# Kernel tuning notes

Measured on AMD Instinct MI355X. Metric: run time of the kernel, lower is better.

## Reference

```python
import jax, jax.numpy as jnp
import numpy as np

B, T, V, H = 32, 2048, 64, 256
HD = H // 2  # per-direction hidden (bidirectional GRU)


def setup_inputs() -> dict:
    key = jax.random.key(0)
    ks = jax.random.split(key, 8)
    s = 0.1
    return {
        "tokens": jax.random.randint(ks[0], (B, T), 0, V, dtype=jnp.int32),
        "lengths": jax.random.randint(ks[1], (B,), 1, T + 1, dtype=jnp.int32),
        "emb": jax.random.normal(ks[2], (V, H), jnp.float32) * s,
        "Wih_f": jax.random.normal(ks[3], (3 * HD, H), jnp.float32) * s,
        "Whh_f": jax.random.normal(ks[4], (3 * HD, HD), jnp.float32) * s,
        "bih_f": jnp.zeros((3 * HD,), jnp.float32),
        "bhh_f": jnp.zeros((3 * HD,), jnp.float32),
        "Wih_b": jax.random.normal(ks[5], (3 * HD, H), jnp.float32) * s,
        "Whh_b": jax.random.normal(ks[6], (3 * HD, HD), jnp.float32) * s,
        "bih_b": jnp.zeros((3 * HD,), jnp.float32),
        "bhh_b": jnp.zeros((3 * HD,), jnp.float32),
    }


def _gru_dir(x, mask, Wih, Whh, bih, bhh):
    # x: [B,T,H] inputs, mask: [B,T] valid positions; torch GRU cell math.
    b, t, _ = x.shape
    hd = Whh.shape[1]
    h0 = jnp.zeros((b, hd), x.dtype)

    def step(h, inp):
        x_t, m_t = inp  # [B,H], [B,1]
        gi = x_t @ Wih.T + bih
        gh = h @ Whh.T + bhh
        gi_r, gi_z, gi_n = jnp.split(gi, 3, axis=-1)
        gh_r, gh_z, gh_n = jnp.split(gh, 3, axis=-1)
        r = jax.nn.sigmoid(gi_r + gh_r)
        z = jax.nn.sigmoid(gi_z + gh_z)
        n = jnp.tanh(gi_n + r * gh_n)
        h_new = (1 - z) * n + z * h
        h = jnp.where(m_t, h_new, h)  # freeze state past sequence end
        return h, h

    _, outs = jax.lax.scan(step, h0, (x.transpose(1, 0, 2), mask.T[:, :, None]))
    return outs.transpose(1, 0, 2)  # [B,T,HD]


def reference(tokens, lengths, emb, Wih_f, Whh_f, bih_f, bhh_f, Wih_b, Whh_b, bih_b, bhh_b):
    lengths = jnp.maximum(lengths, 1)
    x = emb[tokens]  # [B,T,H] embedding lookup
    t_idx = jnp.arange(tokens.shape[1])
    mask = t_idx[None, :] < lengths[:, None]  # [B,T]
    # forward direction
    out_f = _gru_dir(x, mask, Wih_f, Whh_f, bih_f, bhh_f)
    # backward direction: reverse each sequence within its valid region
    ridx = jnp.clip(lengths[:, None] - 1 - t_idx[None, :], 0)  # [B,T]
    x_rev = jnp.take_along_axis(x, ridx[:, :, None], axis=1)
    out_b_rev = _gru_dir(x_rev, mask, Wih_b, Whh_b, bih_b, bhh_b)
    out_b = jnp.take_along_axis(out_b_rev, ridx[:, :, None], axis=1)
    out = jnp.concatenate([out_f, out_b], axis=-1)  # [B,T,H] (torch concat order: fwd, bwd)
    # mean pool over valid timesteps (matches .mean(0) per variable-length sequence)
    denom = lengths[:, None].astype(out.dtype)
    pooled = (out * mask[:, :, None]).sum(axis=1) / denom  # [B,H]
    return pooled
```

## Files before the change

### kernel.cpp

```cpp
#include <hip/hip_runtime.h>

#define BB 32
#define TT 2048
#define VV 64
#define HH 256
#define HD 128
#define G3 384

typedef _Float16 h2 __attribute__((ext_vector_type(2)));
typedef _Float16 h8 __attribute__((ext_vector_type(8)));

__device__ __forceinline__ float fsigmoid(float x) {
  return __builtin_amdgcn_rcpf(1.0f + __expf(-x));
}
__device__ __forceinline__ float ftanh(float x) {
  float ax = fabsf(x);
  float t = __expf(-2.0f * ax);
  float r = 1.0f - 2.0f * t * __builtin_amdgcn_rcpf(1.0f + t);
  return copysignf(r, x);
}

__device__ __forceinline__ float quad_reduce_add(float v) {
  int x = __builtin_amdgcn_mov_dpp(__float_as_int(v), 0xB1, 0xF, 0xF, true);
  v += __int_as_float(x);
  x = __builtin_amdgcn_mov_dpp(__float_as_int(v), 0x4E, 0xF, 0xF, true);
  v += __int_as_float(x);
  return v;
}

template <int D>
__device__ __forceinline__ h2 getpair(h8 v) {
  return __builtin_shufflevector(v, v, 2 * D, 2 * D + 1);
}

__global__ __launch_bounds__(G3, 1)
void gi_table_kernel(const float* __restrict__ emb,
                     const float* __restrict__ Wih_f, const float* __restrict__ bih_f,
                     const float* __restrict__ Wih_b, const float* __restrict__ bih_b,
                     float* __restrict__ gi_ws) {
  const int gid = blockIdx.x;
  const int dir = gid >> 6;
  const int v   = gid & 63;
  const int j   = threadIdx.x;
  const float* Wih = dir ? Wih_b : Wih_f;
  const float* bih = dir ? bih_b : bih_f;
  const float4* er = reinterpret_cast<const float4*>(emb + v * HH);
  const float4* wr = reinterpret_cast<const float4*>(Wih + j * HH);
  float acc = bih[j];
  #pragma unroll 8
  for (int k = 0; k < HH / 4; ++k) {
    float4 e = er[k];
    float4 w = wr[k];
    acc = fmaf(e.x, w.x, acc);
    acc = fmaf(e.y, w.y, acc);
    acc = fmaf(e.z, w.z, acc);
    acc = fmaf(e.w, w.w, acc);
  }
  gi_ws[dir * (VV * G3) + v * G3 + j] = acc;
}

__global__ __launch_bounds__(512, 2)
void gru_kernel(const int* __restrict__ tokens, const int* __restrict__ lengths,
                const float* __restrict__ Whh_f, const float* __restrict__ bhh_f,
                const float* __restrict__ Whh_b, const float* __restrict__ bhh_b,
                const float* __restrict__ gi_ws, float* __restrict__ out) {
  __shared__ float giL[VV * G3];
  __shared__ int   tokL[TT];
  __shared__ __align__(16) _Float16 hbufh[2][HD];

  const int bid  = blockIdx.x;
  const int b    = bid & 31;
  const int dir  = bid >> 5;
  const int tid  = threadIdx.x;
  const int wave = tid >> 6;
  const int lane = tid & 63;
  const int quad = lane >> 2;
  const int p    = lane & 3;
  const int i    = wave * 16 + quad;

  int len = lengths[b];
  if (len < 1) len = 1;

  const float* gi_src = gi_ws + dir * (VV * G3);
  for (int idx = tid; idx < VV * G3; idx += 512) giL[idx] = gi_src[idx];
  const int* tb = tokens + b * TT;
  for (int s = tid; s < len; s += 512) tokL[s] = tb[dir ? (len - 1 - s) : s];
  if (tid < HD) hbufh[0][tid] = (_Float16)0.0f;

  const float* Whh = dir ? Whh_b : Whh_f;
  const float* bhh = dir ? bhh_b : bhh_f;
  h8 w8[3][4];
  #pragma unroll
  for (int g = 0; g < 3; ++g) {
    const float* wr = Whh + (g * HD + i) * HD + p * 32;
    #pragma unroll
    for (int c = 0; c < 4; ++c) {
      const int kb = ((c + p) & 3) * 8;
      h8 w;
      #pragma unroll
      for (int d = 0; d < 8; ++d) w[d] = (_Float16)wr[kb + d];
      w8[g][c] = w;
    }
  }
  const float bhr = bhh[i], bhz = bhh[HD + i], bhn = bhh[2 * HD + i];

  __syncthreads();

  float h = 0.0f, hsum = 0.0f;

  int tok = tokL[0];
  float gir = giL[tok * G3 + i];
  float giz = giL[tok * G3 + HD + i];
  float gin = giL[tok * G3 + 2 * HD + i];

#define DOT8(acc, wv, hv)                                            \
  acc = __builtin_amdgcn_fdot2(getpair<0>(wv), getpair<0>(hv), acc, false); \
  acc = __builtin_amdgcn_fdot2(getpair<1>(wv), getpair<1>(hv), acc, false); \
  acc = __builtin_amdgcn_fdot2(getpair<2>(wv), getpair<2>(hv), acc, false); \
  acc = __builtin_amdgcn_fdot2(getpair<3>(wv), getpair<3>(hv), acc, false)

  #pragma unroll 2
  for (int s = 0; s < len; ++s) {
    const int cur = s & 1;
    const h8* hb8 = reinterpret_cast<const h8*>(&hbufh[cur][0]);

    float accr = bhr, accz = bhz, accn = bhn;
    #pragma unroll
    for (int c = 0; c < 4; ++c) {
      const h8 hv = hb8[p * 4 + ((c + p) & 3)];
      DOT8(accr, w8[0][c], hv);
      DOT8(accz, w8[1][c], hv);
      DOT8(accn, w8[2][c], hv);
    }

    const int sn = (s + 1 < len) ? (s + 1) : 0;
    const int ntok = tokL[sn];
    const float ngir = giL[ntok * G3 + i];
    const float ngiz = giL[ntok * G3 + HD + i];
    const float ngin = giL[ntok * G3 + 2 * HD + i];

    accr = quad_reduce_add(accr);
    accz = quad_reduce_add(accz);
    accn = quad_reduce_add(accn);

    const float r = fsigmoid(gir + accr);
    const float z = fsigmoid(giz + accz);
    const float n = ftanh(gin + r * accn);
    h = (1.0f - z) * n + z * h;
    hsum += h;
    if (p == 0) hbufh[cur ^ 1][i] = (_Float16)h;
    __syncthreads();

    gir = ngir; giz = ngiz; gin = ngin;
  }
#undef DOT8

  if (p == 0) out[b * HH + dir * HD + i] = hsum / (float)len;
}

extern "C" void kernel_launch(void* const* d_in, const int* in_sizes, int n_in,
                              void* d_out, int out_size, void* d_ws, size_t ws_size,
                              hipStream_t stream) {
  const int*   tokens  = (const int*)d_in[0];
  const int*   lengths = (const int*)d_in[1];
  const float* emb     = (const float*)d_in[2];
  const float* Wih_f   = (const float*)d_in[3];
  const float* Whh_f   = (const float*)d_in[4];
  const float* bih_f   = (const float*)d_in[5];
  const float* bhh_f   = (const float*)d_in[6];
  const float* Wih_b   = (const float*)d_in[7];
  const float* Whh_b   = (const float*)d_in[8];
  const float* bih_b   = (const float*)d_in[9];
  const float* bhh_b   = (const float*)d_in[10];
  float* out   = (float*)d_out;
  float* gi_ws = (float*)d_ws;

  gi_table_kernel<<<2 * VV, G3, 0, stream>>>(emb, Wih_f, bih_f, Wih_b, bih_b, gi_ws);
  gru_kernel<<<2 * BB, 512, 0, stream>>>(tokens, lengths, Whh_f, bhh_f, Whh_b, bhh_b,
                                         gi_ws, out);
}
```

Measured before the change: 949.7 us.

## Halve GRU block to 256 threads, two hidden units per quad, prescaled exp2 activations

Each lane quad now computes two hidden units, so the recurrent block shrinks from 512 to 256 threads (4 waves), which makes the per-step barrier cheaper and doubles register-held weights per lane. Input-gate tables, recurrent weights and biases are prescaled by -log2(e) or 2·log2(e), so sigmoid and tanh become raw exp2 plus rcp without extra multiplies. The next-token gate prefetch is pipelined one step further ahead. The cost is twice the dot-product work per lane on the serial critical path and higher register pressure.

```diff
diff --git a/kernel.cpp b/kernel.cpp
--- a/kernel.cpp
+++ b/kernel.cpp
@@ -10,15 +10,8 @@
 typedef _Float16 h2 __attribute__((ext_vector_type(2)));
 typedef _Float16 h8 __attribute__((ext_vector_type(8)));
 
-__device__ __forceinline__ float fsigmoid(float x) {
-  return __builtin_amdgcn_rcpf(1.0f + __expf(-x));
-}
-__device__ __forceinline__ float ftanh(float x) {
-  float ax = fabsf(x);
-  float t = __expf(-2.0f * ax);
-  float r = 1.0f - 2.0f * t * __builtin_amdgcn_rcpf(1.0f + t);
-  return copysignf(r, x);
-}
+#define SRZ (-1.4426950408889634f)
+#define SN  (2.8853900817779268f)
 
 __device__ __forceinline__ float quad_reduce_add(float v) {
   int x = __builtin_amdgcn_mov_dpp(__float_as_int(v), 0xB1, 0xF, 0xF, true);
@@ -56,10 +49,11 @@
     acc = fmaf(e.z, w.z, acc);
     acc = fmaf(e.w, w.w, acc);
   }
-  gi_ws[dir * (VV * G3) + v * G3 + j] = acc;
-}
-
-__global__ __launch_bounds__(512, 2)
+  const float sc = (j < 2 * HD) ? SRZ : SN;
+  gi_ws[dir * (VV * G3) + v * G3 + j] = acc * sc;
+}
+
+__global__ __launch_bounds__(256, 1)
 void gru_kernel(const int* __restrict__ tokens, const int* __restrict__ lengths,
                 const float* __restrict__ Whh_f, const float* __restrict__ bhh_f,
                 const float* __restrict__ Whh_b, const float* __restrict__ bhh_b,
@@ -76,44 +70,53 @@
   const int lane = tid & 63;
   const int quad = lane >> 2;
   const int p    = lane & 3;
-  const int i    = wave * 16 + quad;
+  const int q    = wave * 16 + quad;
+  const int i0   = 2 * q;
 
   int len = lengths[b];
   if (len < 1) len = 1;
 
   const float* gi_src = gi_ws + dir * (VV * G3);
-  for (int idx = tid; idx < VV * G3; idx += 512) giL[idx] = gi_src[idx];
+  for (int idx = tid; idx < VV * G3; idx += 256) giL[idx] = gi_src[idx];
   const int* tb = tokens + b * TT;
-  for (int s = tid; s < len; s += 512) tokL[s] = tb[dir ? (len - 1 - s) : s];
+  for (int s = tid; s < len; s += 256) tokL[s] = tb[dir ? (len - 1 - s) : s];
   if (tid < HD) hbufh[0][tid] = (_Float16)0.0f;
 
   const float* Whh = dir ? Whh_b : Whh_f;
   const float* bhh = dir ? bhh_b : bhh_f;
-  h8 w8[3][4];
+  h8 w8[3][2][4];
   #pragma unroll
   for (int g = 0; g < 3; ++g) {
-    const float* wr = Whh + (g * HD + i) * HD + p * 32;
+    const float sc = (g < 2) ? SRZ : SN;
     #pragma unroll
-    for (int c = 0; c < 4; ++c) {
-      const int kb = ((c + p) & 3) * 8;
-      h8 w;
+    for (int o = 0; o < 2; ++o) {
+      const float* wr = Whh + (g * HD + i0 + o) * HD + p * 32;
       #pragma unroll
-      for (int d = 0; d < 8; ++d) w[d] = (_Float16)wr[kb + d];
-      w8[g][c] = w;
+      for (int c = 0; c < 4; ++c) {
+        const int kb = ((c + p) & 3) * 8;
+        h8 w;
+        #pragma unroll
+        for (int d = 0; d < 8; ++d) w[d] = (_Float16)(wr[kb + d] * sc);
+        w8[g][o][c] = w;
+      }
     }
   }
-  const float bhr = bhh[i], bhz = bhh[HD + i], bhn = bhh[2 * HD + i];
+  const float bhr0 = bhh[i0] * SRZ,          bhr1 = bhh[i0 + 1] * SRZ;
+  const float bhz0 = bhh[HD + i0] * SRZ,     bhz1 = bhh[HD + i0 + 1] * SRZ;
+  const float bhn0 = bhh[2 * HD + i0] * SN,  bhn1 = bhh[2 * HD + i0 + 1] * SN;
 
   __syncthreads();
 
-  float h = 0.0f, hsum = 0.0f;
-
-  int tok = tokL[0];
-  float gir = giL[tok * G3 + i];
-  float giz = giL[tok * G3 + HD + i];
-  float gin = giL[tok * G3 + 2 * HD + i];
-
-#define DOT8(acc, wv, hv)                                            \
+  float h0 = 0.0f, h1 = 0.0f, hsum0 = 0.0f, hsum1 = 0.0f;
+
+  const float2* giL2 = reinterpret_cast<const float2*>(giL);
+  int tok0 = tokL[0];
+  float2 gr = giL2[(tok0 * G3) / 2 + q];
+  float2 gz = giL2[(tok0 * G3 + HD) / 2 + q];
+  float2 gn = giL2[(tok0 * G3 + 2 * HD) / 2 + q];
+  int ntok = tokL[(1 < len) ? 1 : 0];
+
+#define DOT8(acc, wv, hv)                                                   \
   acc = __builtin_amdgcn_fdot2(getpair<0>(wv), getpair<0>(hv), acc, false); \
   acc = __builtin_amdgcn_fdot2(getpair<1>(wv), getpair<1>(hv), acc, false); \
   acc = __builtin_amdgcn_fdot2(getpair<2>(wv), getpair<2>(hv), acc, false); \
@@ -124,38 +127,64 @@
     const int cur = s & 1;
     const h8* hb8 = reinterpret_cast<const h8*>(&hbufh[cur][0]);
 
-    float accr = bhr, accz = bhz, accn = bhn;
-    #pragma unroll
-    for (int c = 0; c < 4; ++c) {
-      const h8 hv = hb8[p * 4 + ((c + p) & 3)];
-      DOT8(accr, w8[0][c], hv);
-      DOT8(accz, w8[1][c], hv);
-      DOT8(accn, w8[2][c], hv);
+    const h8 hv0 = hb8[p * 4 + ((0 + p) & 3)];
+    const h8 hv1 = hb8[p * 4 + ((1 + p) & 3)];
+    const h8 hv2 = hb8[p * 4 + ((2 + p) & 3)];
+    const h8 hv3 = hb8[p * 4 + ((3 + p) & 3)];
+
+    const float2 ngr = giL2[(ntok * G3) / 2 + q];
+    const float2 ngz = giL2[(ntok * G3 + HD) / 2 + q];
+    const float2 ngn = giL2[(ntok * G3 + 2 * HD) / 2 + q];
+    const int s2 = (s + 2 < len) ? (s + 2) : (len - 1);
+    const int nntok = tokL[s2];
+
+    float ar0 = bhr0, ar1 = bhr1, az0 = bhz0, az1 = bhz1, an0 = bhn0, an1 = bhn1;
+    DOT8(ar0, w8[0][0][0], hv0); DOT8(ar1, w8[0][1][0], hv0);
+    DOT8(az0, w8[1][0][0], hv0); DOT8(az1, w8[1][1][0], hv0);
+    DOT8(an0, w8[2][0][0], hv0); DOT8(an1, w8[2][1][0], hv0);
+    DOT8(ar0, w8[0][0][1], hv1); DOT8(ar1, w8[0][1][1], hv1);
+    DOT8(az0, w8[1][0][1], hv1); DOT8(az1, w8[1][1][1], hv1);
+    DOT8(an0, w8[2][0][1], hv1); DOT8(an1, w8[2][1][1], hv1);
+    DOT8(ar0, w8[0][0][2], hv2); DOT8(ar1, w8[0][1][2], hv2);
+    DOT8(az0, w8[1][0][2], hv2); DOT8(az1, w8[1][1][2], hv2);
+    DOT8(an0, w8[2][0][2], hv2); DOT8(an1, w8[2][1][2], hv2);
+    DOT8(ar0, w8[0][0][3], hv3); DOT8(ar1, w8[0][1][3], hv3);
+    DOT8(az0, w8[1][0][3], hv3); DOT8(az1, w8[1][1][3], hv3);
+    DOT8(an0, w8[2][0][3], hv3); DOT8(an1, w8[2][1][3], hv3);
+
+    ar0 = quad_reduce_add(ar0); ar1 = quad_reduce_add(ar1);
+    az0 = quad_reduce_add(az0); az1 = quad_reduce_add(az1);
+    an0 = quad_reduce_add(an0); an1 = quad_reduce_add(an1);
+
+    const float r0 = __builtin_amdgcn_rcpf(1.0f + __builtin_amdgcn_exp2f(gr.x + ar0));
+    const float r1 = __builtin_amdgcn_rcpf(1.0f + __builtin_amdgcn_exp2f(gr.y + ar1));
+    const float z0 = __builtin_amdgcn_rcpf(1.0f + __builtin_amdgcn_exp2f(gz.x + az0));
+    const float z1 = __builtin_amdgcn_rcpf(1.0f + __builtin_amdgcn_exp2f(gz.y + az1));
+    const float n0 = 1.0f - 2.0f * __builtin_amdgcn_rcpf(1.0f + __builtin_amdgcn_exp2f(gn.x + r0 * an0));
+    const float n1 = 1.0f - 2.0f * __builtin_amdgcn_rcpf(1.0f + __builtin_amdgcn_exp2f(gn.y + r1 * an1));
+    h0 = (1.0f - z0) * n0 + z0 * h0;
+    h1 = (1.0f - z1) * n1 + z1 * h1;
+    hsum0 += h0;
+    hsum1 += h1;
+    if (p == 0) {
+      h2 hpk;
+      hpk.x = (_Float16)h0;
+      hpk.y = (_Float16)h1;
+      reinterpret_cast<h2*>(&hbufh[cur ^ 1][0])[q] = hpk;
     }
-
-    const int sn = (s + 1 < len) ? (s + 1) : 0;
-    const int ntok = tokL[sn];
-    const float ngir = giL[ntok * G3 + i];
-    const float ngiz = giL[ntok * G3 + HD + i];
-    const float ngin = giL[ntok * G3 + 2 * HD + i];
-
-    accr = quad_reduce_add(accr);
-    accz = quad_reduce_add(accz);
-    accn = quad_reduce_add(accn);
-
-    const float r = fsigmoid(gir + accr);
-    const float z = fsigmoid(giz + accz);
-    const float n = ftanh(gin + r * accn);
-    h = (1.0f - z) * n + z * h;
-    hsum += h;
-    if (p == 0) hbufh[cur ^ 1][i] = (_Float16)h;
     __syncthreads();
 
-    gir = ngir; giz = ngiz; gin = ngin;
+    gr = ngr; gz = ngz; gn = ngn; ntok = nntok;
   }
 #undef DOT8
 
-  if (p == 0) out[b * HH + dir * HD + i] = hsum / (float)len;
+  if (p == 0) {
+    const float inv = 1.0f / (float)len;
+    float2 o2;
+    o2.x = hsum0 * inv;
+    o2.y = hsum1 * inv;
+    reinterpret_cast<float2*>(out + b * HH + dir * HD)[q] = o2;
+  }
 }
 
 extern "C" void kernel_launch(void* const* d_in, const int* in_sizes, int n_in,
@@ -176,6 +205,6 @@
   float* gi_ws = (float*)d_ws;
 
   gi_table_kernel<<<2 * VV, G3, 0, stream>>>(emb, Wih_f, bih_f, Wih_b, bih_b, gi_ws);
-  gru_kernel<<<2 * BB, 512, 0, stream>>>(tokens, lengths, Whh_f, bhh_f, Whh_b, bhh_b,
+  gru_kernel<<<2 * BB, 256, 0, stream>>>(tokens, lengths, Whh_f, bhh_f, Whh_b, bhh_b,
                                          gi_ws, out);
 }
```

Measured after the change: 852.2 us. -10.3%, faster.

## Halve GRU block to 256 threads with pair-split dots and prescaled exp2 gates

Applied to the files above, without the earlier changes.

Each hidden unit is now computed by two lanes instead of four, with 64-element halves per lane, so the block shrinks to 4 waves and the cross-lane reduction needs one DPP step instead of two. The input and recurrent weights and biases are prescaled by -log2(e) or 2*log2(e), so sigmoid and tanh become a single exp2 plus reciprocal. Token offsets are premultiplied and gate inputs are prefetched two steps ahead. Hidden state is written to two staggered LDS copies so the two half-lanes read from separate regions. The cost is more registers per thread (24 h8 weight vectors) and more serial dot work per lane on each step.

```diff
diff --git a/kernel.cpp b/kernel.cpp
--- a/kernel.cpp
+++ b/kernel.cpp
@@ -10,22 +10,12 @@
 typedef _Float16 h2 __attribute__((ext_vector_type(2)));
 typedef _Float16 h8 __attribute__((ext_vector_type(8)));
 
-__device__ __forceinline__ float fsigmoid(float x) {
-  return __builtin_amdgcn_rcpf(1.0f + __expf(-x));
-}
-__device__ __forceinline__ float ftanh(float x) {
-  float ax = fabsf(x);
-  float t = __expf(-2.0f * ax);
-  float r = 1.0f - 2.0f * t * __builtin_amdgcn_rcpf(1.0f + t);
-  return copysignf(r, x);
-}
+#define SRZ (-1.4426950408889634f)
+#define SN  (2.8853900817779268f)
 
-__device__ __forceinline__ float quad_reduce_add(float v) {
+__device__ __forceinline__ float pair_reduce_add(float v) {
   int x = __builtin_amdgcn_mov_dpp(__float_as_int(v), 0xB1, 0xF, 0xF, true);
-  v += __int_as_float(x);
-  x = __builtin_amdgcn_mov_dpp(__float_as_int(v), 0x4E, 0xF, 0xF, true);
-  v += __int_as_float(x);
-  return v;
+  return v + __int_as_float(x);
 }
 
 template <int D>
@@ -56,17 +46,18 @@
     acc = fmaf(e.z, w.z, acc);
     acc = fmaf(e.w, w.w, acc);
   }
-  gi_ws[dir * (VV * G3) + v * G3 + j] = acc;
+  const float sc = (j < 2 * HD) ? SRZ : SN;
+  gi_ws[dir * (VV * G3) + v * G3 + j] = acc * sc;
 }
 
-__global__ __launch_bounds__(512, 2)
+__global__ __launch_bounds__(256, 1)
 void gru_kernel(const int* __restrict__ tokens, const int* __restrict__ lengths,
                 const float* __restrict__ Whh_f, const float* __restrict__ bhh_f,
                 const float* __restrict__ Whh_b, const float* __restrict__ bhh_b,
                 const float* __restrict__ gi_ws, float* __restrict__ out) {
   __shared__ float giL[VV * G3];
   __shared__ int   tokL[TT];
-  __shared__ __align__(16) _Float16 hbufh[2][HD];
+  __shared__ __align__(16) _Float16 hb[2][2][160];
 
   const int bid  = blockIdx.x;
   const int b    = bid & 31;
@@ -74,46 +65,52 @@
   const int tid  = threadIdx.x;
   const int wave = tid >> 6;
   const int lane = tid & 63;
-  const int quad = lane >> 2;
-  const int p    = lane & 3;
-  const int i    = wave * 16 + quad;
+  const int kh   = lane & 1;
+  const int i    = wave * 32 + (lane >> 1);
 
   int len = lengths[b];
   if (len < 1) len = 1;
 
-  const float* gi_src = gi_ws + dir * (VV * G3);
-  for (int idx = tid; idx < VV * G3; idx += 512) giL[idx] = gi_src[idx];
-  const int* tb = tokens + b * TT;
-  for (int s = tid; s < len; s += 512) tokL[s] = tb[dir ? (len - 1 - s) : s];
-  if (tid < HD) hbufh[0][tid] = (_Float16)0.0f;
+  {
+    const float4* gs = reinterpret_cast<const float4*>(gi_ws + dir * (VV * G3));
+    float4* gd = reinterpret_cast<float4*>(giL);
+    for (int idx = tid; idx < VV * G3 / 4; idx += 256) gd[idx] = gs[idx];
+    const int* tb = tokens + b * TT;
+    for (int s = tid; s < len; s += 256) tokL[s] = tb[dir ? (len - 1 - s) : s] * G3;
+    _Float16* hz = reinterpret_cast<_Float16*>(hb);
+    for (int idx = tid; idx < 2 * 2 * 160; idx += 256) hz[idx] = (_Float16)0.0f;
+  }
 
   const float* Whh = dir ? Whh_b : Whh_f;
   const float* bhh = dir ? bhh_b : bhh_f;
-  h8 w8[3][4];
+  h8 w8[3][8];
   #pragma unroll
   for (int g = 0; g < 3; ++g) {
-    const float* wr = Whh + (g * HD + i) * HD + p * 32;
+    const float sc = (g < 2) ? SRZ : SN;
+    const float* wr = Whh + (g * HD + i) * HD + kh * 64;
     #pragma unroll
-    for (int c = 0; c < 4; ++c) {
-      const int kb = ((c + p) & 3) * 8;
+    for (int c = 0; c < 8; ++c) {
       h8 w;
       #pragma unroll
-      for (int d = 0; d < 8; ++d) w[d] = (_Float16)wr[kb + d];
+      for (int d = 0; d < 8; ++d) w[d] = (_Float16)(wr[c * 8 + d] * sc);
       w8[g][c] = w;
     }
   }
-  const float bhr = bhh[i], bhz = bhh[HD + i], bhn = bhh[2 * HD + i];
+  const float bhr = bhh[i] * SRZ;
+  const float bhz = bhh[HD + i] * SRZ;
+  const float bhn = bhh[2 * HD + i] * SN;
 
   __syncthreads();
 
   float h = 0.0f, hsum = 0.0f;
 
-  int tok = tokL[0];
-  float gir = giL[tok * G3 + i];
-  float giz = giL[tok * G3 + HD + i];
-  float gin = giL[tok * G3 + 2 * HD + i];
+  int tokOff = tokL[0];
+  float gr = giL[tokOff + i];
+  float gz = giL[tokOff + HD + i];
+  float gn = giL[tokOff + 2 * HD + i];
+  int ntokOff = tokL[(1 < len) ? 1 : 0];
 
-#define DOT8(acc, wv, hv)                                            \
+#define DOT8(acc, wv, hv)                                                   \
   acc = __builtin_amdgcn_fdot2(getpair<0>(wv), getpair<0>(hv), acc, false); \
   acc = __builtin_amdgcn_fdot2(getpair<1>(wv), getpair<1>(hv), acc, false); \
   acc = __builtin_amdgcn_fdot2(getpair<2>(wv), getpair<2>(hv), acc, false); \
@@ -122,40 +119,45 @@
   #pragma unroll 2
   for (int s = 0; s < len; ++s) {
     const int cur = s & 1;
-    const h8* hb8 = reinterpret_cast<const h8*>(&hbufh[cur][0]);
+    const h8* hv8 = reinterpret_cast<const h8*>(&hb[cur][kh][kh * 64]);
+    const h8 hv0 = hv8[0], hv1 = hv8[1], hv2 = hv8[2], hv3 = hv8[3];
+    const h8 hv4 = hv8[4], hv5 = hv8[5], hv6 = hv8[6], hv7 = hv8[7];
 
-    float accr = bhr, accz = bhz, accn = bhn;
-    #pragma unroll
-    for (int c = 0; c < 4; ++c) {
-      const h8 hv = hb8[p * 4 + ((c + p) & 3)];
-      DOT8(accr, w8[0][c], hv);
-      DOT8(accz, w8[1][c], hv);
-      DOT8(accn, w8[2][c], hv);
-    }
+    const float ngr = giL[ntokOff + i];
+    const float ngz = giL[ntokOff + HD + i];
+    const float ngn = giL[ntokOff + 2 * HD + i];
+    int s2 = s + 2;
+    if (s2 >= len) s2 = len - 1;
+    const int nnOff = tokL[s2];
 
-    const int sn = (s + 1 < len) ? (s + 1) : 0;
-    const int ntok = tokL[sn];
-    const float ngir = giL[ntok * G3 + i];
-    const float ngiz = giL[ntok * G3 + HD + i];
-    const float ngin = giL[ntok * G3 + 2 * HD + i];
+    float ar = bhr, az = bhz, an = bhn;
+    DOT8(ar, w8[0][0], hv0); DOT8(az, w8[1][0], hv0); DOT8(an, w8[2][0], hv0);
+    DOT8(ar, w8[0][1], hv1); DOT8(az, w8[1][1], hv1); DOT8(an, w8[2][1], hv1);
+    DOT8(ar, w8[0][2], hv2); DOT8(az, w8[1][2], hv2); DOT8(an, w8[2][2], hv2);
+    DOT8(ar, w8[0][3], hv3); DOT8(az, w8[1][3], hv3); DOT8(an, w8[2][3], hv3);
+    DOT8(ar, w8[0][4], hv4); DOT8(az, w8[1][4], hv4); DOT8(an, w8[2][4], hv4);
+    DOT8(ar, w8[0][5], hv5); DOT8(az, w8[1][5], hv5); DOT8(an, w8[2][5], hv5);
+    DOT8(ar, w8[0][6], hv6); DOT8(az, w8[1][6], hv6); DOT8(an, w8[2][6], hv6);
+    DOT8(ar, w8[0][7], hv7); DOT8(az, w8[1][7], hv7); DOT8(an, w8[2][7], hv7);
 
-    accr = quad_reduce_add(accr);
-    accz = quad_reduce_add(accz);
-    accn = quad_reduce_add(accn);
+    ar = pair_reduce_add(ar);
+    az = pair_reduce_add(az);
+    an = pair_reduce_add(an);
 
-    const float r = fsigmoid(gir + accr);
-    const float z = fsigmoid(giz + accz);
-    const float n = ftanh(gin + r * accn);
-    h = (1.0f - z) * n + z * h;
+    const float r = __builtin_amdgcn_rcpf(1.0f + __builtin_amdgcn_exp2f(gr + ar));
+    const float z = __builtin_amdgcn_rcpf(1.0f + __builtin_amdgcn_exp2f(gz + az));
+    const float tn = __builtin_amdgcn_rcpf(1.0f + __builtin_amdgcn_exp2f(fmaf(r, an, gn)));
+    const float n = fmaf(-2.0f, tn, 1.0f);
+    h = fmaf(z, h - n, n);
+    hb[cur ^ 1][kh][i] = (_Float16)h;
     hsum += h;
-    if (p == 0) hbufh[cur ^ 1][i] = (_Float16)h;
     __syncthreads();
 
-    gir = ngir; giz = ngiz; gin = ngin;
+    gr = ngr; gz = ngz; gn = ngn; ntokOff = nnOff;
   }
 #undef DOT8
 
-  if (p == 0) out[b * HH + dir * HD + i] = hsum / (float)len;
+  if (!(lane & 1)) out[b * HH + dir * HD + i] = hsum / (float)len;
 }
 
 extern "C" void kernel_launch(void* const* d_in, const int* in_sizes, int n_in,
@@ -176,6 +178,6 @@
   float* gi_ws = (float*)d_ws;
 
   gi_table_kernel<<<2 * VV, G3, 0, stream>>>(emb, Wih_f, bih_f, Wih_b, bih_b, gi_ws);
-  gru_kernel<<<2 * BB, 512, 0, stream>>>(tokens, lengths, Whh_f, bhh_f, Whh_b, bhh_b,
+  gru_kernel<<<2 * BB, 256, 0, stream>>>(tokens, lengths, Whh_f, bhh_f, Whh_b, bhh_b,
                                          gi_ws, out);
 }
```

Result: faster. 803.8 us (-15.4%).
